# Kernel optimization log

Hardware: AMD Instinct MI355X
Metric: run time of the kernel (lower is better)

Reference implementation:

```python
import jax, jax.numpy as jnp
import numpy as np

B, RES, DIM, H, KD = 16, 32, 768, 12, 64
N = RES * RES          # 1024 tokens
D = KD                 # attn_ratio = 1 -> per-head value dim == key_dim
DH = D * H             # 768
SCALE = KD ** -0.5
LN_EPS = 1e-5


def _bias_idxs():
    # replicate the itertools.product construction: for row-major points,
    # offsets (|dy|,|dx|) are first seen in order dy-major, so id = |dy|*RES + |dx|
    coords = np.arange(N)
    y, x = coords // RES, coords % RES
    dy = np.abs(y[:, None] - y[None, :])
    dx = np.abs(x[:, None] - x[None, :])
    return jnp.asarray(dy * RES + dx, dtype=jnp.int32)  # [N, N]


def setup_inputs() -> dict:
    key = jax.random.key(0)
    ks = jax.random.split(key, 8)
    return {
        "x": jax.random.normal(ks[0], (B, N, DIM), jnp.float32),
        "ln_w": 1.0 + 0.01 * jax.random.normal(ks[1], (DIM,), jnp.float32),
        "ln_b": 0.01 * jax.random.normal(ks[2], (DIM,), jnp.float32),
        "qkv_w": 0.02 * jax.random.normal(ks[3], (3 * H * KD, DIM), jnp.float32),
        "qkv_b": 0.01 * jax.random.normal(ks[4], (3 * H * KD,), jnp.float32),
        "proj_w": 0.02 * jax.random.normal(ks[5], (DIM, DH), jnp.float32),
        "proj_b": 0.01 * jax.random.normal(ks[6], (DIM,), jnp.float32),
        "attn_biases": 0.1 * jax.random.normal(ks[7], (H, RES * RES), jnp.float32),
        "bias_idxs": _bias_idxs(),
    }


def reference(x, ln_w, ln_b, qkv_w, qkv_b, proj_w, proj_b, attn_biases, bias_idxs):
    # LayerNorm over the feature dim
    mu = jnp.mean(x, axis=-1, keepdims=True)
    var = jnp.mean(jnp.square(x - mu), axis=-1, keepdims=True)
    xn = (x - mu) * jax.lax.rsqrt(var + LN_EPS) * ln_w + ln_b

    # fused qkv projection -> [B, N, H, 3*KD], split per head
    qkv = (xn @ qkv_w.T + qkv_b).reshape(B, N, H, 3 * KD)
    q, k, v = jnp.split(qkv, [KD, 2 * KD], axis=3)  # each [B, N, H, KD]

    # gathered relative-position bias: [H, N, N]
    bias = attn_biases[:, bias_idxs]

    # scores + bias -> softmax -> AV
    attn = jnp.einsum("bnhk,bmhk->bhnm", q, k) * SCALE + bias[None]
    attn = jax.nn.softmax(attn, axis=-1)
    out = jnp.einsum("bhnm,bmhd->bnhd", attn, v).reshape(B, N, DH)
    return out @ proj_w.T + proj_b
```

## Files before the change

### kernel.cpp

```cpp
#include <hip/hip_runtime.h>
#include <cstdint>
#include <cstddef>

#define AS1 __attribute__((address_space(1)))
#define AS3 __attribute__((address_space(3)))

typedef float f32x4 __attribute__((ext_vector_type(4)));
typedef __bf16 bf16x8 __attribute__((ext_vector_type(8)));
typedef __bf16 bf16x4 __attribute__((ext_vector_type(4)));
typedef _Float16 h16x4 __attribute__((ext_vector_type(4)));
typedef uint32_t u32x4 __attribute__((ext_vector_type(4)));

__device__ __forceinline__ void async_cp16(void* lds, const void* g) {
    __builtin_amdgcn_global_load_lds((AS1 void*)(g), (AS3 void*)(lds), 16, 0, 0);
}

__device__ __forceinline__ bf16x8 frag_of(u32x4 u) {
    return __builtin_bit_cast(bf16x8, u);
}

__global__ __launch_bounds__(256)
void cvt_w(const float* __restrict__ qkvw, const float* __restrict__ projw,
           __bf16* __restrict__ qkvwb, __bf16* __restrict__ projwb) {
    int i = blockIdx.x * 256 + threadIdx.x;
    if (i < 442368) {
        int row = i / 192, c4 = (i - row * 192) * 4;
        int t = (row >= 1536) ? 2 : (row >= 768 ? 1 : 0);
        int rem = row - t * 768;
        int hh = rem >> 6, d = rem & 63;
        int in_row = hh * 192 + t * 64 + d;
        float4 v = *(const float4*)(qkvw + (long)in_row * 768 + c4);
        bf16x4 o;
        o[0] = (__bf16)v.x; o[1] = (__bf16)v.y; o[2] = (__bf16)v.z; o[3] = (__bf16)v.w;
        *(bf16x4*)(qkvwb + (long)row * 768 + c4) = o;
    } else {
        int j = i - 442368;
        float4 v = ((const float4*)projw)[j];
        bf16x4 o;
        o[0] = (__bf16)v.x; o[1] = (__bf16)v.y; o[2] = (__bf16)v.z; o[3] = (__bf16)v.w;
        ((bf16x4*)projwb)[j] = o;
    }
}

__global__ __launch_bounds__(256)
void ln_kernel(const float* __restrict__ x, const float* __restrict__ w,
               const float* __restrict__ bsh, __bf16* __restrict__ xn) {
    const int lane = threadIdx.x & 63;
    const long row = (long)blockIdx.x * 4 + (threadIdx.x >> 6);
    const float4* xr = (const float4*)(x + row * 768);
    float4 v[3];
    v[0] = xr[lane]; v[1] = xr[lane + 64]; v[2] = xr[lane + 128];
    float s = 0.f, ss = 0.f;
#pragma unroll
    for (int i = 0; i < 3; ++i) {
        s  += v[i].x + v[i].y + v[i].z + v[i].w;
        ss += v[i].x * v[i].x + v[i].y * v[i].y + v[i].z * v[i].z + v[i].w * v[i].w;
    }
#pragma unroll
    for (int m = 1; m < 64; m <<= 1) { s += __shfl_xor(s, m); ss += __shfl_xor(ss, m); }
    const float mean = s * (1.f / 768.f);
    const float rstd = rsqrtf(ss * (1.f / 768.f) - mean * mean + 1e-5f);
    const float4* wv = (const float4*)w;
    const float4* bv = (const float4*)bsh;
    bf16x4* outp = (bf16x4*)(xn + row * 768);
#pragma unroll
    for (int i = 0; i < 3; ++i) {
        float4 wi = wv[lane + 64 * i], bi = bv[lane + 64 * i];
        bf16x4 o;
        o[0] = (__bf16)((v[i].x - mean) * rstd * wi.x + bi.x);
        o[1] = (__bf16)((v[i].y - mean) * rstd * wi.y + bi.y);
        o[2] = (__bf16)((v[i].z - mean) * rstd * wi.z + bi.z);
        o[3] = (__bf16)((v[i].w - mean) * rstd * wi.w + bi.w);
        outp[lane + 64 * i] = o;
    }
}

template <int MODE>
__device__ __forceinline__
void gemm_core(__bf16* As, __bf16* Bs,
               const __bf16* __restrict__ A, const __bf16* __restrict__ Bw,
               const float* __restrict__ bias,
               __bf16* __restrict__ q_out, __bf16* __restrict__ k_out,
               __bf16* __restrict__ vt_out, float* __restrict__ f_out,
               long bm, long bn) {
    constexpr int K = 768;
    const int tid  = threadIdx.x;
    const int lane = tid & 63;
    const int quad = lane >> 4;
    const int l16  = lane & 15;
    const int wave = tid >> 6;
    const int wm = wave >> 1, wn = wave & 1;

    const __bf16* Ab = A  + bm * K;
    const __bf16* Bb = Bw + bn * K;

    const int el0 = tid, el1 = tid + 256;
    const int rA0 = el0 >> 2, rA1 = el1 >> 2;
    const int kc  = (tid & 3) * 8;

    f32x4 acc[4][4] = {};

    for (int k0 = 0; k0 < K; k0 += 32) {
        __syncthreads();
        async_cp16((char*)As + el0 * 16, Ab + (long)rA0 * K + (k0 + kc));
        async_cp16((char*)As + el1 * 16, Ab + (long)rA1 * K + (k0 + kc));
        async_cp16((char*)Bs + el0 * 16, Bb + (long)rA0 * K + (k0 + kc));
        async_cp16((char*)Bs + el1 * 16, Bb + (long)rA1 * K + (k0 + kc));
        __syncthreads();

        const u32x4* Av = (const u32x4*)As;
        const u32x4* Bv = (const u32x4*)Bs;
        bf16x8 af[4], bfr[4];
#pragma unroll
        for (int t = 0; t < 4; ++t) {
            af[t]  = frag_of(Av[(wm * 64 + t * 16 + l16) * 4 + quad]);
            bfr[t] = frag_of(Bv[(wn * 64 + t * 16 + l16) * 4 + quad]);
        }
#pragma unroll
        for (int i = 0; i < 4; ++i)
#pragma unroll
            for (int j = 0; j < 4; ++j) {
                if constexpr (MODE == 0)
                    acc[i][j] = __builtin_amdgcn_mfma_f32_16x16x32_bf16(bfr[j], af[i], acc[i][j], 0, 0, 0);
                else
                    acc[i][j] = __builtin_amdgcn_mfma_f32_16x16x32_bf16(af[i], bfr[j], acc[i][j], 0, 0, 0);
            }
    }

    if constexpr (MODE == 0) {
#pragma unroll
        for (int j = 0; j < 4; ++j) {
            int col0 = (int)bn + wn * 64 + j * 16 + quad * 4;
            int t  = col0 >= 768;
            int cc = col0 - t * 768;
            int h  = cc >> 6, d = cc & 63;
            int f  = h * 192 + t * 64 + d;
            float4 bb = *(const float4*)(bias + f);
            __bf16* dst = t ? k_out : q_out;
#pragma unroll
            for (int i = 0; i < 4; ++i) {
                long row = bm + wm * 64 + i * 16 + l16;
                long b   = row >> 10;
                long n   = row & 1023;
                bf16x4 pk;
                pk[0] = (__bf16)(acc[i][j][0] + bb.x);
                pk[1] = (__bf16)(acc[i][j][1] + bb.y);
                pk[2] = (__bf16)(acc[i][j][2] + bb.z);
                pk[3] = (__bf16)(acc[i][j][3] + bb.w);
                *(bf16x4*)(dst + ((b * 12 + h) * 1024 + n) * 64 + d) = pk;
            }
        }
    } else if constexpr (MODE == 2) {
#pragma unroll
        for (int j = 0; j < 4; ++j) {
            int cv = (int)bn - 1536 + wn * 64 + j * 16 + l16;
            int h  = cv >> 6, d = cv & 63;
            float bv = bias[h * 192 + 128 + d];
#pragma unroll
            for (int i = 0; i < 4; ++i) {
                long row0 = bm + wm * 64 + i * 16 + quad * 4;
                long b    = row0 >> 10;
                long n0   = row0 & 1023;
                bf16x4 pk;
                pk[0] = (__bf16)(acc[i][j][0] + bv);
                pk[1] = (__bf16)(acc[i][j][1] + bv);
                pk[2] = (__bf16)(acc[i][j][2] + bv);
                pk[3] = (__bf16)(acc[i][j][3] + bv);
                *(bf16x4*)(vt_out + ((b * 12 + h) * 64 + d) * 1024 + n0) = pk;
            }
        }
    } else {
#pragma unroll
        for (int i = 0; i < 4; ++i) {
#pragma unroll
            for (int r = 0; r < 4; ++r) {
                long row = bm + wm * 64 + i * 16 + quad * 4 + r;
#pragma unroll
                for (int j = 0; j < 4; ++j) {
                    int col = (int)bn + wn * 64 + j * 16 + l16;
                    f_out[row * 768 + col] = acc[i][j][r] + bias[col];
                }
            }
        }
    }
}

__global__ __launch_bounds__(256, 3)
void gemm_qkv(const __bf16* __restrict__ A, const __bf16* __restrict__ Bw,
              const float* __restrict__ bias, __bf16* __restrict__ qb,
              __bf16* __restrict__ kb, __bf16* __restrict__ vtb) {
    __shared__ __align__(16) __bf16 As[128 * 32];
    __shared__ __align__(16) __bf16 Bs[128 * 32];
    int blk  = blockIdx.x;
    int xcd  = blk & 7;
    int rest = blk >> 3;
    int bx   = rest % 18;
    int byg  = rest / 18;
    long by  = xcd + 8 * byg;
    if (bx < 12)
        gemm_core<0>(As, Bs, A, Bw, bias, qb, kb, nullptr, nullptr, by * 128, (long)bx * 128);
    else
        gemm_core<2>(As, Bs, A, Bw, bias, nullptr, nullptr, vtb, nullptr, by * 128, (long)bx * 128);
}

__global__ __launch_bounds__(256, 3)
void gemm_proj(const __bf16* __restrict__ A, const __bf16* __restrict__ Bw,
               const float* __restrict__ bias, float* __restrict__ out) {
    __shared__ __align__(16) __bf16 As[128 * 32];
    __shared__ __align__(16) __bf16 Bs[128 * 32];
    int blk  = blockIdx.x;
    int xcd  = blk & 7;
    int rest = blk >> 3;
    int bx   = rest % 6;
    int byg  = rest / 6;
    long by  = xcd + 8 * byg;
    gemm_core<1>(As, Bs, A, Bw, bias, nullptr, nullptr, nullptr, out,
                 by * 128, (long)bx * 128);
}

__global__ __launch_bounds__(512, 6)
void attn_kernel(const __bf16* __restrict__ Q, const __bf16* __restrict__ Kb,
                 const __bf16* __restrict__ Vt, const float* __restrict__ biases,
                 __bf16* __restrict__ out) {
    __shared__ __align__(16) __bf16 QPs[128 * 64];
    __shared__ __align__(16) __bf16 Ks[2][64 * 64];
    __shared__ __align__(16) __bf16 Vts[2][64 * 64];
    __shared__ __align__(16) float brow[1024];

    const int tid  = threadIdx.x;
    const int lane = tid & 63;
    const int wave = tid >> 6;
    const int quad = lane >> 4;
    const int l16  = lane & 15;
    const int sw   = l16 & 7;

    int blk  = blockIdx.x;
    int xcd  = blk & 7;
    int rest = blk >> 3;
    int qt   = rest & 7;
    int bhg  = rest >> 3;
    int bh_i = xcd + 8 * bhg;
    int b    = bh_i / 12;
    int h    = bh_i - b * 12;

    const long bh = bh_i;
    const __bf16* Qg  = Q  + (bh * 1024 + qt * 128) * 64;
    const __bf16* Kg  = Kb + bh * 1024 * 64;
    const __bf16* Vtg = Vt + bh * 64 * 1024;

    {
        const int e0 = tid, e1 = tid + 512;
        const int r0 = e0 >> 3, c0 = (e0 & 7) ^ (r0 & 7);
        const int r1 = e1 >> 3, c1 = (e1 & 7) ^ (r1 & 7);
        async_cp16((char*)QPs + e0 * 16, Qg + r0 * 64 + c0 * 8);
        async_cp16((char*)QPs + e1 * 16, Qg + r1 * 64 + c1 * 8);
    }
    const int rk = tid >> 3;
    const int ck = (tid & 7) ^ (rk & 7);
    async_cp16((char*)Ks[0]  + tid * 16, Kg  + rk * 64   + ck * 8);
    async_cp16((char*)Vts[0] + tid * 16, Vtg + rk * 1024 + ck * 8);
    {
        const float LOG2E = 1.4426950408889634f;
        float2 v = ((const float2*)(biases + (long)h * 1024))[tid];
        float2 o; o.x = v.x * LOG2E; o.y = v.y * LOG2E;
        *(float2*)(brow + tid * 2) = o;
    }
    __syncthreads();

    bf16x8 aq[2];
    {
        const u32x4* Qv = (const u32x4*)QPs;
        int qrow = wave * 16 + l16;
        aq[0] = frag_of(Qv[qrow * 8 + (quad ^ sw)]);
        aq[1] = frag_of(Qv[qrow * 8 + ((quad + 4) ^ sw)]);
    }

    const int yq = 4 * qt + (wave >> 1);
    const int xq = ((wave & 1) << 4) + l16;
    int pdx[2][4];
#pragma unroll
    for (int i2 = 0; i2 < 2; ++i2)
#pragma unroll
        for (int r = 0; r < 4; ++r) {
            int xk = (i2 << 4) + quad * 4 + r;
            int d = xq - xk; pdx[i2][r] = d < 0 ? -d : d;
        }

    const float SSCALE = 0.125f * 1.4426950408889634f;
    float lacc = 0.f;
    f32x4 o[4] = {};
    __bf16* Psw = QPs + wave * 1024;
    const int pwb = l16 * 128 + (quad & 1) * 8;

    for (int kt = 0; kt < 16; ++kt) {
        const int cb = kt & 1;
        if (kt < 15) {
            const int nb = cb ^ 1;
            const __bf16* Kt  = Kg  + (kt + 1) * 4096;
            const __bf16* Vtt = Vtg + (kt + 1) * 64;
            async_cp16((char*)Ks[nb]  + tid * 16, Kt  + rk * 64   + ck * 8);
            async_cp16((char*)Vts[nb] + tid * 16, Vtt + rk * 1024 + ck * 8);
        }

        f32x4 s[4];
        const u32x4* Kv = (const u32x4*)Ks[cb];
#pragma unroll
        for (int nt = 0; nt < 4; ++nt) {
            int krow = nt * 16 + l16;
            bf16x8 k0 = frag_of(Kv[krow * 8 + (quad ^ sw)]);
            bf16x8 k1 = frag_of(Kv[krow * 8 + ((quad + 4) ^ sw)]);
            f32x4 z = {0.f, 0.f, 0.f, 0.f};
            z = __builtin_amdgcn_mfma_f32_16x16x32_bf16(k0, aq[0], z, 0, 0, 0);
            z = __builtin_amdgcn_mfma_f32_16x16x32_bf16(k1, aq[1], z, 0, 0, 0);
            s[nt] = z;
        }

        int dy0 = yq - 2 * kt;     dy0 = dy0 < 0 ? -dy0 : dy0;
        int dy1 = yq - 2 * kt - 1; dy1 = dy1 < 0 ? -dy1 : dy1;
        const float* br0 = brow + dy0 * 32;
        const float* br1 = brow + dy1 * 32;
#pragma unroll
        for (int nt = 0; nt < 4; ++nt) {
            const float* br = (nt & 2) ? br1 : br0;
            bf16x4 pk;
#pragma unroll
            for (int r = 0; r < 4; ++r) {
                float p = __builtin_amdgcn_exp2f(s[nt][r] * SSCALE + br[pdx[nt & 1][r]]);
                lacc += p;
                pk[r] = (__bf16)p;
            }
            *(bf16x4*)((char*)Psw + pwb + (((nt * 2 + (quad >> 1)) ^ sw) << 4)) = pk;
        }

        const u32x4* Pv = (const u32x4*)Psw;
        const u32x4* Vv = (const u32x4*)Vts[cb];
        bf16x8 bp0 = frag_of(Pv[l16 * 8 + (quad ^ sw)]);
        bf16x8 bp1 = frag_of(Pv[l16 * 8 + ((quad + 4) ^ sw)]);
#pragma unroll
        for (int dt = 0; dt < 4; ++dt) {
            int vrow = dt * 16 + l16;
            bf16x8 v0 = frag_of(Vv[vrow * 8 + (quad ^ sw)]);
            bf16x8 v1 = frag_of(Vv[vrow * 8 + ((quad + 4) ^ sw)]);
            o[dt] = __builtin_amdgcn_mfma_f32_16x16x32_bf16(v0, bp0, o[dt], 0, 0, 0);
            o[dt] = __builtin_amdgcn_mfma_f32_16x16x32_bf16(v1, bp1, o[dt], 0, 0, 0);
        }

        __syncthreads();
    }

    lacc += __shfl_xor(lacc, 16);
    lacc += __shfl_xor(lacc, 32);
    const float rl = 1.f / lacc;

    const long n = qt * 128 + wave * 16 + l16;
    __bf16* op = out + ((long)b * 1024 + n) * 768 + h * 64 + quad * 4;
#pragma unroll
    for (int dt = 0; dt < 4; ++dt) {
        bf16x4 ov;
        ov[0] = (__bf16)(o[dt][0] * rl);
        ov[1] = (__bf16)(o[dt][1] * rl);
        ov[2] = (__bf16)(o[dt][2] * rl);
        ov[3] = (__bf16)(o[dt][3] * rl);
        *(bf16x4*)(op + dt * 16) = ov;
    }
}

extern "C" void kernel_launch(void* const* d_in, const int* in_sizes, int n_in,
                              void* d_out, int out_size, void* d_ws, size_t ws_size,
                              hipStream_t stream) {
    (void)in_sizes; (void)n_in; (void)out_size; (void)ws_size;
    const float* x      = (const float*)d_in[0];
    const float* ln_w   = (const float*)d_in[1];
    const float* ln_b   = (const float*)d_in[2];
    const float* qkv_w  = (const float*)d_in[3];
    const float* qkv_b  = (const float*)d_in[4];
    const float* proj_w = (const float*)d_in[5];
    const float* proj_b = (const float*)d_in[6];
    const float* ab     = (const float*)d_in[7];
    float* outp = (float*)d_out;

    char* ws = (char*)d_ws;
    __bf16* xn     = (__bf16*)(ws);
    __bf16* aout   = (__bf16*)(ws);
    __bf16* qkvwb  = (__bf16*)(ws + 25165824);
    __bf16* projwb = (__bf16*)(ws + 28704768);
    __bf16* qb     = (__bf16*)(ws + 29884416);
    __bf16* kb     = (__bf16*)(ws + 55050240);
    __bf16* vtb    = (__bf16*)(ws + 80216064);

    cvt_w<<<2304, 256, 0, stream>>>(qkv_w, proj_w, qkvwb, projwb);
    ln_kernel<<<4096, 256, 0, stream>>>(x, ln_w, ln_b, xn);
    gemm_qkv<<<2304, 256, 0, stream>>>(xn, qkvwb, qkv_b, qb, kb, vtb);
    attn_kernel<<<1536, 512, 0, stream>>>(qb, kb, vtb, ab, aout);
    gemm_proj<<<768, 256, 0, stream>>>(aout, projwb, proj_b, outp);
}
```

Measured before the change: 311.0 us.

## Rewrite QKV GEMM as 256x256 tile with 4-stage async LDS pipeline

Replaces the 128x128 single-buffered QKV GEMM with a 256x256-tile kernel using 512 threads and a 4-deep ring of LDS buffers. Global-to-LDS async copies run three k-steps ahead, guarded by vmcnt waits, so loads overlap MFMA work. The LDS layout is XOR-swizzled to reduce bank conflicts, and s_setprio is raised around the MFMA block. It uses 128KB of dynamic shared memory per block and more accumulator registers, which reduces occupancy and adds correctness risk in the hand-written wait counts.

```diff
diff --git a/kernel.cpp b/kernel.cpp
--- a/kernel.cpp
+++ b/kernel.cpp
@@ -75,14 +75,145 @@
     }
 }
 
-template <int MODE>
+template <int SWAP>
 __device__ __forceinline__
-void gemm_core(__bf16* As, __bf16* Bs,
-               const __bf16* __restrict__ A, const __bf16* __restrict__ Bw,
-               const float* __restrict__ bias,
-               __bf16* __restrict__ q_out, __bf16* __restrict__ k_out,
-               __bf16* __restrict__ vt_out, float* __restrict__ f_out,
-               long bm, long bn) {
+void gemm256_body(char* smem, const __bf16* __restrict__ A,
+                  const __bf16* __restrict__ Bw, const float* __restrict__ bias,
+                  __bf16* __restrict__ q_out, __bf16* __restrict__ k_out,
+                  __bf16* __restrict__ vt_out, long bm, long bn) {
+    const int tid  = threadIdx.x;
+    const int lane = tid & 63;
+    const int quad = lane >> 4;
+    const int l16  = lane & 15;
+    const int wave = tid >> 6;
+    const int wm = wave >> 2, wn = wave & 3;
+
+    const __bf16* Ag = A  + bm * 768;
+    const __bf16* Bg = Bw + bn * 768;
+    const int r0  = tid >> 2;
+    const int sc  = ((tid & 3) ^ ((tid >> 3) & 3)) * 8;
+    const int swq = quad ^ ((l16 >> 1) & 3);
+
+    f32x4 acc[8][4] = {};
+
+    auto stage = [&](int t) {
+        char* base = smem + (size_t)(t & 3) * 32768;
+        const __bf16* As_ = Ag + t * 32 + sc;
+        const __bf16* Bs_ = Bg + t * 32 + sc;
+        async_cp16(base + tid * 16,                 As_ + (size_t)r0 * 768);
+        async_cp16(base + (tid + 512) * 16,         As_ + (size_t)(r0 + 128) * 768);
+        async_cp16(base + 16384 + tid * 16,         Bs_ + (size_t)r0 * 768);
+        async_cp16(base + 16384 + (tid + 512) * 16, Bs_ + (size_t)(r0 + 128) * 768);
+    };
+
+    auto kstep = [&](int buf) {
+        const u32x4* Ab = (const u32x4*)(smem + (size_t)buf * 32768);
+        const u32x4* Bb = (const u32x4*)(smem + (size_t)buf * 32768 + 16384);
+        bf16x8 af[8], bfv[4];
+#pragma unroll
+        for (int m = 0; m < 8; ++m)
+            af[m] = frag_of(Ab[(wm * 128 + m * 16 + l16) * 4 + swq]);
+#pragma unroll
+        for (int n = 0; n < 4; ++n)
+            bfv[n] = frag_of(Bb[(wn * 64 + n * 16 + l16) * 4 + swq]);
+        __builtin_amdgcn_s_setprio(1);
+#pragma unroll
+        for (int m = 0; m < 8; ++m)
+#pragma unroll
+            for (int n = 0; n < 4; ++n) {
+                if constexpr (SWAP)
+                    acc[m][n] = __builtin_amdgcn_mfma_f32_16x16x32_bf16(bfv[n], af[m], acc[m][n], 0, 0, 0);
+                else
+                    acc[m][n] = __builtin_amdgcn_mfma_f32_16x16x32_bf16(af[m], bfv[n], acc[m][n], 0, 0, 0);
+            }
+        __builtin_amdgcn_s_setprio(0);
+    };
+
+    stage(0); stage(1); stage(2);
+    for (int t = 0; t < 21; ++t) {
+        asm volatile("s_waitcnt vmcnt(8)" ::: "memory");
+        __builtin_amdgcn_s_barrier();
+        stage(t + 3);
+        kstep(t & 3);
+    }
+    asm volatile("s_waitcnt vmcnt(8)" ::: "memory");
+    __builtin_amdgcn_s_barrier();
+    kstep(1);
+    asm volatile("s_waitcnt vmcnt(4)" ::: "memory");
+    __builtin_amdgcn_s_barrier();
+    kstep(2);
+    asm volatile("s_waitcnt vmcnt(0)" ::: "memory");
+    __builtin_amdgcn_s_barrier();
+    kstep(3);
+
+    if constexpr (SWAP) {
+#pragma unroll
+        for (int n = 0; n < 4; ++n) {
+            int col0 = (int)bn + wn * 64 + n * 16 + quad * 4;
+            int t_ = col0 >= 768;
+            int cc = col0 - t_ * 768;
+            int hh = cc >> 6, dd = cc & 63;
+            int f  = hh * 192 + t_ * 64 + dd;
+            float4 bb = *(const float4*)(bias + f);
+            __bf16* dst = t_ ? k_out : q_out;
+#pragma unroll
+            for (int m = 0; m < 8; ++m) {
+                long row = bm + wm * 128 + m * 16 + l16;
+                long b   = row >> 10;
+                long nn  = row & 1023;
+                bf16x4 pk;
+                pk[0] = (__bf16)(acc[m][n][0] + bb.x);
+                pk[1] = (__bf16)(acc[m][n][1] + bb.y);
+                pk[2] = (__bf16)(acc[m][n][2] + bb.z);
+                pk[3] = (__bf16)(acc[m][n][3] + bb.w);
+                *(bf16x4*)(dst + ((b * 12 + hh) * 1024 + nn) * 64 + dd) = pk;
+            }
+        }
+    } else {
+#pragma unroll
+        for (int n = 0; n < 4; ++n) {
+            int cv = (int)bn - 1536 + wn * 64 + n * 16 + l16;
+            int hh = cv >> 6, dd = cv & 63;
+            float bv = bias[hh * 192 + 128 + dd];
+#pragma unroll
+            for (int m = 0; m < 8; ++m) {
+                long row0 = bm + wm * 128 + m * 16 + quad * 4;
+                long b    = row0 >> 10;
+                long n0   = row0 & 1023;
+                bf16x4 pk;
+                pk[0] = (__bf16)(acc[m][n][0] + bv);
+                pk[1] = (__bf16)(acc[m][n][1] + bv);
+                pk[2] = (__bf16)(acc[m][n][2] + bv);
+                pk[3] = (__bf16)(acc[m][n][3] + bv);
+                *(bf16x4*)(vt_out + ((b * 12 + hh) * 64 + dd) * 1024 + n0) = pk;
+            }
+        }
+    }
+}
+
+__global__ __launch_bounds__(512, 2)
+void gemm_qkv(const __bf16* __restrict__ A, const __bf16* __restrict__ Bw,
+              const float* __restrict__ bias, __bf16* __restrict__ qb,
+              __bf16* __restrict__ kb, __bf16* __restrict__ vtb) {
+    extern __shared__ char smem[];
+    int blk  = blockIdx.x;
+    int xcd  = blk & 7;
+    int rest = blk >> 3;
+    int bx   = rest % 9;
+    int byg  = rest / 9;
+    long by  = xcd + 8 * byg;
+    long bm  = by * 256, bn = (long)bx * 256;
+    if (bx < 6)
+        gemm256_body<1>(smem, A, Bw, bias, qb, kb, nullptr, bm, bn);
+    else
+        gemm256_body<0>(smem, A, Bw, bias, nullptr, nullptr, vtb, bm, bn);
+}
+
+__device__ __forceinline__
+void gemm_core1(__bf16* As, __bf16* Bs,
+                const __bf16* __restrict__ A, const __bf16* __restrict__ Bw,
+                const float* __restrict__ bias, float* __restrict__ f_out,
+                long bm, long bn) {
     constexpr int K = 768;
     const int tid  = threadIdx.x;
     const int lane = tid & 63;
@@ -119,88 +250,22 @@
 #pragma unroll
         for (int i = 0; i < 4; ++i)
 #pragma unroll
+            for (int j = 0; j < 4; ++j)
+                acc[i][j] = __builtin_amdgcn_mfma_f32_16x16x32_bf16(af[i], bfr[j], acc[i][j], 0, 0, 0);
+    }
+
+#pragma unroll
+    for (int i = 0; i < 4; ++i) {
+#pragma unroll
+        for (int r = 0; r < 4; ++r) {
+            long row = bm + wm * 64 + i * 16 + quad * 4 + r;
+#pragma unroll
             for (int j = 0; j < 4; ++j) {
-                if constexpr (MODE == 0)
-                    acc[i][j] = __builtin_amdgcn_mfma_f32_16x16x32_bf16(bfr[j], af[i], acc[i][j], 0, 0, 0);
-                else
-                    acc[i][j] = __builtin_amdgcn_mfma_f32_16x16x32_bf16(af[i], bfr[j], acc[i][j], 0, 0, 0);
+                int col = (int)bn + wn * 64 + j * 16 + l16;
+                f_out[row * 768 + col] = acc[i][j][r] + bias[col];
             }
-    }
-
-    if constexpr (MODE == 0) {
-#pragma unroll
-        for (int j = 0; j < 4; ++j) {
-            int col0 = (int)bn + wn * 64 + j * 16 + quad * 4;
-            int t  = col0 >= 768;
-            int cc = col0 - t * 768;
-            int h  = cc >> 6, d = cc & 63;
-            int f  = h * 192 + t * 64 + d;
-            float4 bb = *(const float4*)(bias + f);
-            __bf16* dst = t ? k_out : q_out;
-#pragma unroll
-            for (int i = 0; i < 4; ++i) {
-                long row = bm + wm * 64 + i * 16 + l16;
-                long b   = row >> 10;
-                long n   = row & 1023;
-                bf16x4 pk;
-                pk[0] = (__bf16)(acc[i][j][0] + bb.x);
-                pk[1] = (__bf16)(acc[i][j][1] + bb.y);
-                pk[2] = (__bf16)(acc[i][j][2] + bb.z);
-                pk[3] = (__bf16)(acc[i][j][3] + bb.w);
-                *(bf16x4*)(dst + ((b * 12 + h) * 1024 + n) * 64 + d) = pk;
-            }
-        }
-    } else if constexpr (MODE == 2) {
-#pragma unroll
-        for (int j = 0; j < 4; ++j) {
-            int cv = (int)bn - 1536 + wn * 64 + j * 16 + l16;
-            int h  = cv >> 6, d = cv & 63;
-            float bv = bias[h * 192 + 128 + d];
-#pragma unroll
-            for (int i = 0; i < 4; ++i) {
-                long row0 = bm + wm * 64 + i * 16 + quad * 4;
-                long b    = row0 >> 10;
-                long n0   = row0 & 1023;
-                bf16x4 pk;
-                pk[0] = (__bf16)(acc[i][j][0] + bv);
-                pk[1] = (__bf16)(acc[i][j][1] + bv);
-                pk[2] = (__bf16)(acc[i][j][2] + bv);
-                pk[3] = (__bf16)(acc[i][j][3] + bv);
-                *(bf16x4*)(vt_out + ((b * 12 + h) * 64 + d) * 1024 + n0) = pk;
-            }
-        }
-    } else {
-#pragma unroll
-        for (int i = 0; i < 4; ++i) {
-#pragma unroll
-            for (int r = 0; r < 4; ++r) {
-                long row = bm + wm * 64 + i * 16 + quad * 4 + r;
-#pragma unroll
-                for (int j = 0; j < 4; ++j) {
-                    int col = (int)bn + wn * 64 + j * 16 + l16;
-                    f_out[row * 768 + col] = acc[i][j][r] + bias[col];
-                }
-            }
-        }
-    }
-}
-
-__global__ __launch_bounds__(256, 3)
-void gemm_qkv(const __bf16* __restrict__ A, const __bf16* __restrict__ Bw,
-              const float* __restrict__ bias, __bf16* __restrict__ qb,
-              __bf16* __restrict__ kb, __bf16* __restrict__ vtb) {
-    __shared__ __align__(16) __bf16 As[128 * 32];
-    __shared__ __align__(16) __bf16 Bs[128 * 32];
-    int blk  = blockIdx.x;
-    int xcd  = blk & 7;
-    int rest = blk >> 3;
-    int bx   = rest % 18;
-    int byg  = rest / 18;
-    long by  = xcd + 8 * byg;
-    if (bx < 12)
-        gemm_core<0>(As, Bs, A, Bw, bias, qb, kb, nullptr, nullptr, by * 128, (long)bx * 128);
-    else
-        gemm_core<2>(As, Bs, A, Bw, bias, nullptr, nullptr, vtb, nullptr, by * 128, (long)bx * 128);
+        }
+    }
 }
 
 __global__ __launch_bounds__(256, 3)
@@ -214,8 +279,7 @@
     int bx   = rest % 6;
     int byg  = rest / 6;
     long by  = xcd + 8 * byg;
-    gemm_core<1>(As, Bs, A, Bw, bias, nullptr, nullptr, nullptr, out,
-                 by * 128, (long)bx * 128);
+    gemm_core1(As, Bs, A, Bw, bias, out, by * 128, (long)bx * 128);
 }
 
 __global__ __launch_bounds__(512, 6)
@@ -390,7 +454,7 @@
 
     cvt_w<<<2304, 256, 0, stream>>>(qkv_w, proj_w, qkvwb, projwb);
     ln_kernel<<<4096, 256, 0, stream>>>(x, ln_w, ln_b, xn);
-    gemm_qkv<<<2304, 256, 0, stream>>>(xn, qkvwb, qkv_b, qb, kb, vtb);
+    gemm_qkv<<<576, 512, 131072, stream>>>(xn, qkvwb, qkv_b, qb, kb, vtb);
     attn_kernel<<<1536, 512, 0, stream>>>(qb, kb, vtb, ab, aout);
     gemm_proj<<<768, 256, 0, stream>>>(aout, projwb, proj_b, outp);
 }
```

Measured after the change: 323.2 us. 1.04x slower.
